# Kernel optimization log

Hardware: AMD Instinct MI355X
Metric: run time of the kernel (lower is better)

The kernel has to match this reference:

```python
import jax, jax.numpy as jnp
import numpy as np

N_THRESHOLDS = 10


def setup_inputs() -> dict:
    key = jax.random.key(0)
    k1, k2, k3 = jax.random.split(key, 3)
    shape = (32, 1024, 1024)
    prediction = jax.random.normal(k1, shape, dtype=jnp.float32)
    mask = jax.random.randint(k2, shape, 0, 2, dtype=jnp.int32)
    target = jax.random.randint(k3, shape, 0, 2, dtype=jnp.int32)
    return {"prediction": prediction, "mask": mask, "target": target}


def reference(prediction, mask, target):
    # thresholds = linspace(0,1,n+2)[1:-1], same as the torch module
    thresholds = jnp.linspace(0.0, 1.0, N_THRESHOLDS + 2, dtype=jnp.float32)[1:-1]

    s = jax.nn.sigmoid(prediction).ravel()            # [N]
    m = mask.ravel().astype(bool)                     # [N] valid mask
    t = target.ravel().astype(bool)                   # [N]
    mt = m & t                                        # masked positives

    # Broadcast compare against all thresholds at once (single fused pass,
    # no per-threshold host sync like the original loop).
    pos = s[None, :] > thresholds[:, None]            # [T, N] bool

    tp = jnp.sum(pos & mt[None, :], axis=1)           # [T] int32
    p = jnp.sum(pos & m[None, :], axis=1)             # predicted-positive count

    total_m = jnp.sum(m)                              # total valid elements
    total_t = jnp.sum(mt)                             # total true positives in mask

    fp = p - tp
    fn = total_t - tp
    tn = total_m - p - fn

    # classes layout matches torch module: rows = [tp, fp, tn, fn]
    return jnp.stack([tp, fp, tn, fn], axis=0).astype(jnp.float32)
```

## Files before the change

### kernel.cpp

```cpp
#include <hip/hip_runtime.h>


#define NTHR 10
#define NBKT 11
#define NCNT 22
#define WS_STRIDE 16

typedef unsigned long long u64;
typedef unsigned u32;
typedef float __attribute__((ext_vector_type(4))) f32x4;
typedef int   __attribute__((ext_vector_type(4))) i32x4;

__device__ __forceinline__ unsigned wave_reduce_add(unsigned v) {
#pragma unroll
    for (int off = 32; off > 0; off >>= 1)
        v += __shfl_down(v, off, 64);
    return v;
}

__global__ __launch_bounds__(64) void zero_ws_kernel(u32* __restrict__ ws) {
    int i = threadIdx.x;
    if (i < NCNT) ws[i * WS_STRIDE] = 0u;
}

__device__ __forceinline__ void acc_elem(float x, u32 mm, u32 tt, u64& hP, u64& hT) {
    u32 mt = mm & tt;
    float e = __expf(-x);
    float s = __builtin_amdgcn_rcpf(1.0f + e);
    int bi = (int)(s * 11.0f);
    u32 b = (u32)(bi > 10 ? 10 : bi);
    u32 sh = b * 5u;
    hP += (u64)mm << sh;
    hT += (u64)mt << sh;
}

__device__ __forceinline__ void acc_vec(const f32x4& p, const i32x4& m, const i32x4& t,
                                        u64& hP, u64& hT) {
    acc_elem(p.x, (u32)m.x, (u32)t.x, hP, hT);
    acc_elem(p.y, (u32)m.y, (u32)t.y, hP, hT);
    acc_elem(p.z, (u32)m.z, (u32)t.z, hP, hT);
    acc_elem(p.w, (u32)m.w, (u32)t.w, hP, hT);
}

__device__ __forceinline__ void flush_hist(u64& hP, u64& hT,
                                           u64& Plo, u64& Phi, u64& Tlo, u64& Thi) {
#pragma unroll
    for (int b = 0; b < 6; ++b) {
        Plo += (u64)((u32)(hP >> (5 * b)) & 31u) << (10 * b);
        Tlo += (u64)((u32)(hT >> (5 * b)) & 31u) << (10 * b);
    }
#pragma unroll
    for (int b = 6; b < NBKT; ++b) {
        Phi += (u64)((u32)(hP >> (5 * b)) & 31u) << (10 * (b - 6));
        Thi += (u64)((u32)(hT >> (5 * b)) & 31u) << (10 * (b - 6));
    }
    hP = 0ull; hT = 0ull;
}

__device__ __forceinline__ f32x4 zf4() { f32x4 v; v.x = v.y = v.z = v.w = 0.0f; return v; }
__device__ __forceinline__ i32x4 zi4() { i32x4 v; v.x = v.y = v.z = v.w = 0;    return v; }

#define NTL(p) __builtin_nontemporal_load(p)

#define LOAD_BATCH(S, b)                                                      \
    do {                                                                      \
        if ((b) + 256 <= nvec) {                                              \
            S##p0 = NTL(pred4 + (b) +       lane);                            \
            S##p1 = NTL(pred4 + (b) +  64 + lane);                            \
            S##p2 = NTL(pred4 + (b) + 128 + lane);                            \
            S##p3 = NTL(pred4 + (b) + 192 + lane);                            \
            S##m0 = NTL(mask4 + (b) +       lane);                            \
            S##m1 = NTL(mask4 + (b) +  64 + lane);                            \
            S##m2 = NTL(mask4 + (b) + 128 + lane);                            \
            S##m3 = NTL(mask4 + (b) + 192 + lane);                            \
            S##t0 = NTL(targ4 + (b) +       lane);                            \
            S##t1 = NTL(targ4 + (b) +  64 + lane);                            \
            S##t2 = NTL(targ4 + (b) + 128 + lane);                            \
            S##t3 = NTL(targ4 + (b) + 192 + lane);                            \
        } else {                                                              \
            int g0 = (b) +       lane;                                        \
            int g1 = (b) +  64 + lane;                                        \
            int g2 = (b) + 128 + lane;                                        \
            int g3 = (b) + 192 + lane;                                        \
            if (g0 < nvec) { S##p0 = NTL(pred4 + g0); S##m0 = NTL(mask4 + g0);\
                             S##t0 = NTL(targ4 + g0); }                       \
            else           { S##p0 = zf4(); S##m0 = zi4(); S##t0 = zi4(); }   \
            if (g1 < nvec) { S##p1 = NTL(pred4 + g1); S##m1 = NTL(mask4 + g1);\
                             S##t1 = NTL(targ4 + g1); }                       \
            else           { S##p1 = zf4(); S##m1 = zi4(); S##t1 = zi4(); }   \
            if (g2 < nvec) { S##p2 = NTL(pred4 + g2); S##m2 = NTL(mask4 + g2);\
                             S##t2 = NTL(targ4 + g2); }                       \
            else           { S##p2 = zf4(); S##m2 = zi4(); S##t2 = zi4(); }   \
            if (g3 < nvec) { S##p3 = NTL(pred4 + g3); S##m3 = NTL(mask4 + g3);\
                             S##t3 = NTL(targ4 + g3); }                       \
            else           { S##p3 = zf4(); S##m3 = zi4(); S##t3 = zi4(); }   \
        }                                                                     \
    } while (0)

#define CONSUME_BATCH(S)                                                      \
    do {                                                                      \
        u64 hP = 0ull, hT = 0ull;                                             \
        acc_vec(S##p0, S##m0, S##t0, hP, hT);                                 \
        acc_vec(S##p1, S##m1, S##t1, hP, hT);                                 \
        acc_vec(S##p2, S##m2, S##t2, hP, hT);                                 \
        acc_vec(S##p3, S##m3, S##t3, hP, hT);                                 \
        flush_hist(hP, hT, Plo, Phi, Tlo, Thi);                               \
    } while (0)

__global__ __launch_bounds__(256) void count_kernel(
        const f32x4* __restrict__ pred4,
        const i32x4* __restrict__ mask4,
        const i32x4* __restrict__ targ4,
        const float* __restrict__ pred,
        const int*   __restrict__ mask,
        const int*   __restrict__ targ,
        u32* __restrict__ ws, int nvec, int n) {
    u64 Plo = 0ull, Phi = 0ull, Tlo = 0ull, Thi = 0ull;

    const int tid    = blockIdx.x * blockDim.x + threadIdx.x;
    const int lane   = tid & 63;
    const int waveId = tid >> 6;
    const int totalWaves = (gridDim.x * blockDim.x) >> 6;
    const int strideG    = totalWaves << 8;

    {
        f32x4 Ap0, Ap1, Ap2, Ap3, Bp0, Bp1, Bp2, Bp3;
        i32x4 Am0, Am1, Am2, Am3, Bm0, Bm1, Bm2, Bm3;
        i32x4 At0, At1, At2, At3, Bt0, Bt1, Bt2, Bt3;

        int base = waveId << 8;
        if (base < nvec) {
            LOAD_BATCH(A, base);
            for (;;) {
                int nb = base + strideG;
                bool more = nb < nvec;
                if (more) LOAD_BATCH(B, nb);
                CONSUME_BATCH(A);
                if (!more) break;
                base = nb;

                nb = base + strideG;
                more = nb < nvec;
                if (more) LOAD_BATCH(A, nb);
                CONSUME_BATCH(B);
                if (!more) break;
                base = nb;
            }
        }
    }

    {
        int i = nvec * 4 + tid;
        if (i < n) {
            u64 hP = 0ull, hT = 0ull;
            acc_elem(pred[i], (u32)mask[i], (u32)targ[i], hP, hT);
            flush_hist(hP, hT, Plo, Phi, Tlo, Thi);
        }
    }

    u32 vals[NCNT];
#pragma unroll
    for (int b = 0; b < 6; ++b) {
        vals[b]        = (u32)(Plo >> (10 * b)) & 1023u;
        vals[NBKT + b] = (u32)(Tlo >> (10 * b)) & 1023u;
    }
#pragma unroll
    for (int b = 6; b < NBKT; ++b) {
        vals[b]        = (u32)(Phi >> (10 * (b - 6))) & 1023u;
        vals[NBKT + b] = (u32)(Thi >> (10 * (b - 6))) & 1023u;
    }
#pragma unroll
    for (int c = 0; c < NCNT; ++c) vals[c] = wave_reduce_add(vals[c]);

    __shared__ u32 partial[4][NCNT];
    const int wave = threadIdx.x >> 6;
    if ((threadIdx.x & 63) == 0) {
#pragma unroll
        for (int c = 0; c < NCNT; ++c) partial[wave][c] = vals[c];
    }
    __syncthreads();
    if (threadIdx.x < NCNT) {
        u32 s = partial[0][threadIdx.x] + partial[1][threadIdx.x] +
                partial[2][threadIdx.x] + partial[3][threadIdx.x];
        atomicAdd(&ws[threadIdx.x * WS_STRIDE], s);
    }
}

__global__ __launch_bounds__(64) void finalize_kernel(const u32* __restrict__ ws,
                                                      float* __restrict__ out) {
    int j = threadIdx.x;
    if (j < NTHR) {
        u32 totM = 0u, totT = 0u, p = 0u, tp = 0u;
#pragma unroll
        for (int b = 0; b < NBKT; ++b) {
            u32 vP = ws[b * WS_STRIDE];
            u32 vT = ws[(NBKT + b) * WS_STRIDE];
            totM += vP; totT += vT;
            if (b > j) { p += vP; tp += vT; }
        }
        u32 fp = p - tp;
        u32 fn = totT - tp;
        u32 tn = totM - p - fn;
        out[j]            = (float)tp;
        out[NTHR + j]     = (float)fp;
        out[2 * NTHR + j] = (float)tn;
        out[3 * NTHR + j] = (float)fn;
    }
}

extern "C" void kernel_launch(void* const* d_in, const int* in_sizes, int n_in,
                              void* d_out, int out_size, void* d_ws, size_t ws_size,
                              hipStream_t stream) {
    const float* pred = (const float*)d_in[0];
    const int*   mask = (const int*)d_in[1];
    const int*   targ = (const int*)d_in[2];
    u32*         ws   = (u32*)d_ws;
    float*       out  = (float*)d_out;

    const int n    = in_sizes[0];
    const int nvec = n / 4;

    zero_ws_kernel<<<1, 64, 0, stream>>>(ws);

    const int blocks = 1024;
    count_kernel<<<blocks, 256, 0, stream>>>(
        (const f32x4*)pred, (const i32x4*)mask, (const i32x4*)targ,
        pred, mask, targ, ws, nvec, n);

    finalize_kernel<<<1, 64, 0, stream>>>(ws, out);
}
```

Measured before the change: 330.2 us.

## Deepen load pipeline to four rotating half-size batches in count kernel

Each batch now covers 128 vectors instead of 256, and four register batch sets (A-D) rotate so three batches stay in flight while one is consumed, replacing the two-stage double buffer. The aim is to keep more memory requests outstanding per wave and hide HBM latency on this bandwidth-bound streaming reduction. The total register footprint for loads is unchanged, but the histogram is now flushed twice as often, which adds ALU work, and the loop has more branches.

```diff
diff --git a/kernel.cpp b/kernel.cpp
--- a/kernel.cpp
+++ b/kernel.cpp
@@ -64,36 +64,22 @@
 
 #define LOAD_BATCH(S, b)                                                      \
     do {                                                                      \
-        if ((b) + 256 <= nvec) {                                              \
-            S##p0 = NTL(pred4 + (b) +       lane);                            \
-            S##p1 = NTL(pred4 + (b) +  64 + lane);                            \
-            S##p2 = NTL(pred4 + (b) + 128 + lane);                            \
-            S##p3 = NTL(pred4 + (b) + 192 + lane);                            \
-            S##m0 = NTL(mask4 + (b) +       lane);                            \
-            S##m1 = NTL(mask4 + (b) +  64 + lane);                            \
-            S##m2 = NTL(mask4 + (b) + 128 + lane);                            \
-            S##m3 = NTL(mask4 + (b) + 192 + lane);                            \
-            S##t0 = NTL(targ4 + (b) +       lane);                            \
-            S##t1 = NTL(targ4 + (b) +  64 + lane);                            \
-            S##t2 = NTL(targ4 + (b) + 128 + lane);                            \
-            S##t3 = NTL(targ4 + (b) + 192 + lane);                            \
+        if ((b) + 128 <= nvec) {                                              \
+            S##p0 = NTL(pred4 + (b) +      lane);                             \
+            S##p1 = NTL(pred4 + (b) + 64 + lane);                             \
+            S##m0 = NTL(mask4 + (b) +      lane);                             \
+            S##m1 = NTL(mask4 + (b) + 64 + lane);                             \
+            S##t0 = NTL(targ4 + (b) +      lane);                             \
+            S##t1 = NTL(targ4 + (b) + 64 + lane);                             \
         } else {                                                              \
-            int g0 = (b) +       lane;                                        \
-            int g1 = (b) +  64 + lane;                                        \
-            int g2 = (b) + 128 + lane;                                        \
-            int g3 = (b) + 192 + lane;                                        \
+            int g0 = (b) +      lane;                                         \
+            int g1 = (b) + 64 + lane;                                         \
             if (g0 < nvec) { S##p0 = NTL(pred4 + g0); S##m0 = NTL(mask4 + g0);\
                              S##t0 = NTL(targ4 + g0); }                       \
             else           { S##p0 = zf4(); S##m0 = zi4(); S##t0 = zi4(); }   \
             if (g1 < nvec) { S##p1 = NTL(pred4 + g1); S##m1 = NTL(mask4 + g1);\
                              S##t1 = NTL(targ4 + g1); }                       \
             else           { S##p1 = zf4(); S##m1 = zi4(); S##t1 = zi4(); }   \
-            if (g2 < nvec) { S##p2 = NTL(pred4 + g2); S##m2 = NTL(mask4 + g2);\
-                             S##t2 = NTL(targ4 + g2); }                       \
-            else           { S##p2 = zf4(); S##m2 = zi4(); S##t2 = zi4(); }   \
-            if (g3 < nvec) { S##p3 = NTL(pred4 + g3); S##m3 = NTL(mask4 + g3);\
-                             S##t3 = NTL(targ4 + g3); }                       \
-            else           { S##p3 = zf4(); S##m3 = zi4(); S##t3 = zi4(); }   \
         }                                                                     \
     } while (0)
 
@@ -102,8 +88,6 @@
         u64 hP = 0ull, hT = 0ull;                                             \
         acc_vec(S##p0, S##m0, S##t0, hP, hT);                                 \
         acc_vec(S##p1, S##m1, S##t1, hP, hT);                                 \
-        acc_vec(S##p2, S##m2, S##t2, hP, hT);                                 \
-        acc_vec(S##p3, S##m3, S##t3, hP, hT);                                 \
         flush_hist(hP, hT, Plo, Phi, Tlo, Thi);                               \
     } while (0)
 
@@ -121,30 +105,42 @@
     const int lane   = tid & 63;
     const int waveId = tid >> 6;
     const int totalWaves = (gridDim.x * blockDim.x) >> 6;
-    const int strideG    = totalWaves << 8;
+    const int strideB    = totalWaves << 7;
 
     {
-        f32x4 Ap0, Ap1, Ap2, Ap3, Bp0, Bp1, Bp2, Bp3;
-        i32x4 Am0, Am1, Am2, Am3, Bm0, Bm1, Bm2, Bm3;
-        i32x4 At0, At1, At2, At3, Bt0, Bt1, Bt2, Bt3;
-
-        int base = waveId << 8;
-        if (base < nvec) {
-            LOAD_BATCH(A, base);
+        f32x4 Ap0, Ap1, Bp0, Bp1, Cp0, Cp1, Dp0, Dp1;
+        i32x4 Am0, Am1, Bm0, Bm1, Cm0, Cm1, Dm0, Dm1;
+        i32x4 At0, At1, Bt0, Bt1, Ct0, Ct1, Dt0, Dt1;
+
+        int h = waveId << 7;
+        if (h < nvec) {
+            LOAD_BATCH(A, h);
+            if (h + strideB < nvec)     LOAD_BATCH(B, h + strideB);
+            if (h + 2 * strideB < nvec) LOAD_BATCH(C, h + 2 * strideB);
             for (;;) {
-                int nb = base + strideG;
-                bool more = nb < nvec;
-                if (more) LOAD_BATCH(B, nb);
+                int nb = h + 3 * strideB;
+                if (nb < nvec) LOAD_BATCH(D, nb);
                 CONSUME_BATCH(A);
-                if (!more) break;
-                base = nb;
-
-                nb = base + strideG;
-                more = nb < nvec;
-                if (more) LOAD_BATCH(A, nb);
+                h += strideB;
+                if (h >= nvec) break;
+
+                nb = h + 3 * strideB;
+                if (nb < nvec) LOAD_BATCH(A, nb);
                 CONSUME_BATCH(B);
-                if (!more) break;
-                base = nb;
+                h += strideB;
+                if (h >= nvec) break;
+
+                nb = h + 3 * strideB;
+                if (nb < nvec) LOAD_BATCH(B, nb);
+                CONSUME_BATCH(C);
+                h += strideB;
+                if (h >= nvec) break;
+
+                nb = h + 3 * strideB;
+                if (nb < nvec) LOAD_BATCH(C, nb);
+                CONSUME_BATCH(D);
+                h += strideB;
+                if (h >= nvec) break;
             }
         }
     }
```

Result: no change. 331.4 us (+0.4%).
